# Performance work log

Hardware: AMD Instinct MI355X
Metric: run time of the kernel (lower is better)

Reference implementation:

```python
import jax, jax.numpy as jnp
import numpy as np

D = 1024      # hidden_size
H = 16        # num_heads
HD = D // H   # head_dim = 64
FF = 4096     # intermediate_size
DEPTH = 2
S = 2048      # packed sequence length
NSEG = 4     # number of image segments
EPS = 1e-6


def setup_inputs() -> dict:
    key = jax.random.key(0)
    ks = jax.random.split(key, 8)
    hidden_states = jax.random.normal(ks[0], (S, D), jnp.float32)
    cu_seqlens = jnp.arange(NSEG + 1, dtype=jnp.int32) * (S // NSEG)
    # rotary embedding like RiceRotaryEmbedding(head_dim//2): freqs of dim HD//4
    # per spatial axis, h/w concatenated -> HD//2, then duplicated -> HD
    inv_freq = 1.0 / (10000.0 ** (jnp.arange(0, HD // 2, 2, dtype=jnp.float32) / (HD // 2)))
    pos = jnp.arange(S, dtype=jnp.float32)
    freqs = jnp.outer(pos, inv_freq)                       # [S, HD//4]
    emb = jnp.concatenate([freqs] * 4, axis=-1)            # [S, HD]
    cos, sin = jnp.cos(emb), jnp.sin(emb)

    def w(k, shape, fan):
        return jax.random.normal(k, shape, jnp.float32) / np.sqrt(fan)

    return {
        "hidden_states": hidden_states,
        "cu_seqlens": cu_seqlens,
        "cos": cos,
        "sin": sin,
        "ln1_g": jnp.ones((DEPTH, D), jnp.float32),
        "ln1_b": jnp.zeros((DEPTH, D), jnp.float32),
        "qkv_w": w(ks[1], (DEPTH, D, 3 * D), D),
        "qkv_b": jnp.zeros((DEPTH, 3 * D), jnp.float32),
        "proj_w": w(ks[2], (DEPTH, D, D), D),
        "proj_b": jnp.zeros((DEPTH, D), jnp.float32),
        "ln2_g": jnp.ones((DEPTH, D), jnp.float32),
        "ln2_b": jnp.zeros((DEPTH, D), jnp.float32),
        "fc1_w": w(ks[3], (DEPTH, D, FF), D),
        "fc1_b": jnp.zeros((DEPTH, FF), jnp.float32),
        "fc2_w": w(ks[4], (DEPTH, FF, D), FF),
        "fc2_b": jnp.zeros((DEPTH, D), jnp.float32),
    }


def _ln(x, g, b):
    m = jnp.mean(x, axis=-1, keepdims=True)
    v = jnp.mean(jnp.square(x - m), axis=-1, keepdims=True)
    return (x - m) / jnp.sqrt(v + EPS) * g + b


def _rotate_half(x):
    x1, x2 = jnp.split(x, 2, axis=-1)
    return jnp.concatenate([-x2, x1], axis=-1)


def reference(hidden_states, cu_seqlens, cos, sin,
              ln1_g, ln1_b, qkv_w, qkv_b, proj_w, proj_b,
              ln2_g, ln2_b, fc1_w, fc1_b, fc2_w, fc2_b):
    S_, D_ = hidden_states.shape
    # segment id per token from cu_seqlens -> block-diagonal additive mask
    seg = jnp.searchsorted(cu_seqlens[1:], jnp.arange(S_, dtype=jnp.int32), side="right")
    neg = jnp.finfo(jnp.float32).min
    bias = jnp.where(seg[:, None] == seg[None, :], 0.0, neg)   # [S, S]
    cos_e = cos[:, None, :]  # broadcast over heads, [S,1,HD]
    sin_e = sin[:, None, :]
    scale = 1.0 / np.sqrt(HD)

    x = hidden_states
    for i in range(DEPTH):
        # --- attention ---
        h = _ln(x, ln1_g[i], ln1_b[i])
        qkv = h @ qkv_w[i] + qkv_b[i]                           # [S, 3D]
        q, k, v = [t.reshape(S_, H, HD) for t in jnp.split(qkv, 3, axis=-1)]
        q = q * cos_e + _rotate_half(q) * sin_e
        k = k * cos_e + _rotate_half(k) * sin_e
        scores = jnp.einsum("shd,thd->hst", q, k) * scale + bias  # [H,S,S]
        w_ = jax.nn.softmax(scores.astype(jnp.float32), axis=-1)
        ao = jnp.einsum("hst,thd->shd", w_, v).reshape(S_, D_)
        x = x + ao @ proj_w[i] + proj_b[i]
        # --- mlp ---
        h2 = _ln(x, ln2_g[i], ln2_b[i])
        x = x + jax.nn.gelu(h2 @ fc1_w[i] + fc1_b[i], approximate=False) @ fc2_w[i] + fc2_b[i]
    return x
```

## Files before the change

kernel.cpp:

```cpp
#include <hip/hip_runtime.h>
#include <hip/hip_bf16.h>
#include <math.h>

#define Dm 1024
#define Hn 16
#define HDm 64
#define FFm 4096
#define Sn 2048
#define SEG 512
#define EPSV 1e-6f

typedef __attribute__((ext_vector_type(4))) float f32x4;
typedef __attribute__((ext_vector_type(8))) short s16x8;
typedef __attribute__((ext_vector_type(4))) short s16x4;

__device__ inline short f2bf(float f) {
  __hip_bfloat16 h = __float2bfloat16(f);
  short s;
  __builtin_memcpy(&s, &h, 2);
  return s;
}
__device__ inline float bf2f(short s) {
  unsigned u = ((unsigned)(unsigned short)s) << 16;
  float f;
  __builtin_memcpy(&f, &u, 4);
  return f;
}

__device__ inline float wred_sum(float v) {
#pragma unroll
  for (int m = 32; m > 0; m >>= 1) v += __shfl_xor(v, m, 64);
  return v;
}
__device__ inline float wred_max(float v) {
#pragma unroll
  for (int m = 32; m > 0; m >>= 1) v = fmaxf(v, __shfl_xor(v, m, 64));
  return v;
}

__device__ inline void gld16(const short* g, short* lds_base) {
  __builtin_amdgcn_global_load_lds(
      (const __attribute__((address_space(1))) void*)g,
      (__attribute__((address_space(3))) void*)lds_base, 16, 0, 0);
}

__global__ __launch_bounds__(256) void ln_kernel(const float* __restrict__ x,
                                                 const float* __restrict__ g,
                                                 const float* __restrict__ b,
                                                 short* __restrict__ out) {
  const int row = blockIdx.x;
  const int tid = threadIdx.x;
  f32x4 v = *reinterpret_cast<const f32x4*>(x + (size_t)row * Dm + tid * 4);
  float s1 = v.x + v.y + v.z + v.w;
  float s2 = v.x * v.x + v.y * v.y + v.z * v.z + v.w * v.w;
  s1 = wred_sum(s1);
  s2 = wred_sum(s2);
  __shared__ float t1[4], t2[4];
  if ((tid & 63) == 0) { t1[tid >> 6] = s1; t2[tid >> 6] = s2; }
  __syncthreads();
  s1 = t1[0] + t1[1] + t1[2] + t1[3];
  s2 = t2[0] + t2[1] + t2[2] + t2[3];
  const float mean = s1 * (1.0f / Dm);
  const float var = s2 * (1.0f / Dm) - mean * mean;
  const float rstd = rsqrtf(var + EPSV);
  f32x4 gv = *reinterpret_cast<const f32x4*>(g + tid * 4);
  f32x4 bv = *reinterpret_cast<const f32x4*>(b + tid * 4);
  s16x4 o;
#pragma unroll
  for (int j = 0; j < 4; ++j)
    o[j] = f2bf((v[j] - mean) * rstd * gv[j] + bv[j]);
  *reinterpret_cast<s16x4*>(out + (size_t)row * Dm + tid * 4) = o;
}

template <int SPLIT>
__global__ __launch_bounds__(256) void redln_kernel(const float* __restrict__ pb,
                                                    const float* __restrict__ bias,
                                                    const float* __restrict__ res,
                                                    const float* __restrict__ g,
                                                    const float* __restrict__ b,
                                                    float* __restrict__ xout,
                                                    short* __restrict__ h) {
  const int row = blockIdx.x;
  const int tid = threadIdx.x;
  const size_t idx = (size_t)row * Dm + tid * 4;
  f32x4 o = *reinterpret_cast<const f32x4*>(res + idx);
  o += *reinterpret_cast<const f32x4*>(bias + tid * 4);
#pragma unroll
  for (int s = 0; s < SPLIT; ++s)
    o += *reinterpret_cast<const f32x4*>(pb + (size_t)s * Sn * Dm + idx);
  *reinterpret_cast<f32x4*>(xout + idx) = o;
  float s1 = o.x + o.y + o.z + o.w;
  float s2 = o.x * o.x + o.y * o.y + o.z * o.z + o.w * o.w;
  s1 = wred_sum(s1);
  s2 = wred_sum(s2);
  __shared__ float t1[4], t2[4];
  if ((tid & 63) == 0) { t1[tid >> 6] = s1; t2[tid >> 6] = s2; }
  __syncthreads();
  s1 = t1[0] + t1[1] + t1[2] + t1[3];
  s2 = t2[0] + t2[1] + t2[2] + t2[3];
  const float mean = s1 * (1.0f / Dm);
  const float var = s2 * (1.0f / Dm) - mean * mean;
  const float rstd = rsqrtf(var + EPSV);
  f32x4 gv = *reinterpret_cast<const f32x4*>(g + tid * 4);
  f32x4 bv = *reinterpret_cast<const f32x4*>(b + tid * 4);
  s16x4 ho;
#pragma unroll
  for (int j = 0; j < 4; ++j)
    ho[j] = f2bf((o[j] - mean) * rstd * gv[j] + bv[j]);
  *reinterpret_cast<s16x4*>(h + idx) = ho;
}

template <int SPLIT>
__global__ __launch_bounds__(256) void redln_bf(const short* __restrict__ pb,
                                                const float* __restrict__ bias,
                                                const float* __restrict__ res,
                                                const float* __restrict__ g,
                                                const float* __restrict__ b,
                                                float* __restrict__ xout,
                                                short* __restrict__ h) {
  const int row = blockIdx.x;
  const int tid = threadIdx.x;
  const size_t idx = (size_t)row * Dm + tid * 4;
  f32x4 o = *reinterpret_cast<const f32x4*>(res + idx);
  o += *reinterpret_cast<const f32x4*>(bias + tid * 4);
#pragma unroll
  for (int s = 0; s < SPLIT; ++s) {
    s16x4 v = *reinterpret_cast<const s16x4*>(pb + (size_t)s * Sn * Dm + idx);
#pragma unroll
    for (int j = 0; j < 4; ++j) o[j] += bf2f(v[j]);
  }
  *reinterpret_cast<f32x4*>(xout + idx) = o;
  float s1 = o.x + o.y + o.z + o.w;
  float s2 = o.x * o.x + o.y * o.y + o.z * o.z + o.w * o.w;
  s1 = wred_sum(s1);
  s2 = wred_sum(s2);
  __shared__ float t1[4], t2[4];
  if ((tid & 63) == 0) { t1[tid >> 6] = s1; t2[tid >> 6] = s2; }
  __syncthreads();
  s1 = t1[0] + t1[1] + t1[2] + t1[3];
  s2 = t2[0] + t2[1] + t2[2] + t2[3];
  const float mean = s1 * (1.0f / Dm);
  const float var = s2 * (1.0f / Dm) - mean * mean;
  const float rstd = rsqrtf(var + EPSV);
  f32x4 gv = *reinterpret_cast<const f32x4*>(g + tid * 4);
  f32x4 bv = *reinterpret_cast<const f32x4*>(b + tid * 4);
  s16x4 ho;
#pragma unroll
  for (int j = 0; j < 4; ++j)
    ho[j] = f2bf((o[j] - mean) * rstd * gv[j] + bv[j]);
  *reinterpret_cast<s16x4*>(h + idx) = ho;
}

template <int SPLIT>
__global__ __launch_bounds__(256) void fcred_bf(const short* __restrict__ pb,
                                                const float* __restrict__ bias,
                                                const float* __restrict__ res,
                                                float* __restrict__ out) {
  const size_t i = ((size_t)blockIdx.x * 256 + threadIdx.x) * 4;
  f32x4 o = *reinterpret_cast<const f32x4*>(res + i);
  o += *reinterpret_cast<const f32x4*>(bias + (i & (Dm - 1)));
#pragma unroll
  for (int s = 0; s < SPLIT; ++s) {
    s16x4 v = *reinterpret_cast<const s16x4*>(pb + (size_t)s * Sn * Dm + i);
#pragma unroll
    for (int j = 0; j < 4; ++j) o[j] += bf2f(v[j]);
  }
  *reinterpret_cast<f32x4*>(out + i) = o;
}

__global__ __launch_bounds__(256) void wt_kernel(const float* __restrict__ W,
                                                 short* __restrict__ Wt,
                                                 int K, int N, int ldw) {
  __shared__ float t[32][33];
  const int n0 = blockIdx.x * 32, k0 = blockIdx.y * 32;
  const int tx = threadIdx.x & 31, ty = threadIdx.x >> 5;
#pragma unroll
  for (int r = 0; r < 32; r += 8)
    t[r + ty][tx] = W[(size_t)(k0 + r + ty) * ldw + n0 + tx];
  __syncthreads();
#pragma unroll
  for (int r = 0; r < 32; r += 8)
    Wt[(size_t)(n0 + r + ty) * K + k0 + tx] = f2bf(t[tx][r + ty]);
}

__global__ __launch_bounds__(256) void wtb_kernel(const short* __restrict__ V,
                                                  short* __restrict__ Vt,
                                                  int K, int N, int ldv) {
  __shared__ short t[32][34];
  const int n0 = blockIdx.x * 32, k0 = blockIdx.y * 32;
  const int tx = threadIdx.x & 31, ty = threadIdx.x >> 5;
#pragma unroll
  for (int r = 0; r < 32; r += 8)
    t[r + ty][tx] = V[(size_t)(k0 + r + ty) * ldv + n0 + tx];
  __syncthreads();
#pragma unroll
  for (int r = 0; r < 32; r += 8)
    Vt[(size_t)(n0 + r + ty) * K + k0 + tx] = t[tx][r + ty];
}

__global__ __launch_bounds__(512) void qksoft_kernel(const short* __restrict__ qkvb,
                                                     short* __restrict__ probs) {
  __shared__ short Qs[128 * 64];
  __shared__ short Ks[512 * 64];
  __shared__ float red[128][4];
  const int tid = threadIdx.x;
  const int lane = tid & 63;
  const int wave = tid >> 6;
  const int wm = wave >> 2, wn = wave & 3;
  const int l15 = lane & 15, lg = lane >> 4, rx = l15 & 7;
  const int qblk = blockIdx.x;
  const int z = blockIdx.y;
  const int seg = z & 3, head = z >> 2;

  const int srow = tid >> 3;
  const int sch = ((tid & 7) ^ (srow & 7)) * 8;

  const short* Qg = qkvb + (size_t)(seg * SEG + qblk * 128 + srow) * 3072 +
                    head * HDm + sch;
  const short* Kg = qkvb + (size_t)(seg * SEG + srow) * 3072 + Dm +
                    head * HDm + sch;
#pragma unroll
  for (int j = 0; j < 2; ++j)
    gld16(Qg + (size_t)(j * 64) * 3072, &Qs[(j * 64 + wave * 8) * 64]);
#pragma unroll
  for (int j = 0; j < 8; ++j)
    gld16(Kg + (size_t)(j * 64) * 3072, &Ks[(j * 64 + wave * 8) * 64]);
  __syncthreads();

  f32x4 acc[4][8] = {};
#pragma unroll
  for (int kc = 0; kc < 8; kc += 4) {
    s16x8 af[4], bf8[8];
#pragma unroll
    for (int f = 0; f < 4; ++f)
      af[f] = *reinterpret_cast<const s16x8*>(
          &Qs[(wm * 64 + f * 16 + l15) * 64 + (((lg + kc) ^ rx) << 3)]);
#pragma unroll
    for (int f = 0; f < 8; ++f)
      bf8[f] = *reinterpret_cast<const s16x8*>(
          &Ks[(wn * 128 + f * 16 + l15) * 64 + (((lg + kc) ^ rx) << 3)]);
#pragma unroll
    for (int fi = 0; fi < 4; ++fi)
#pragma unroll
      for (int fj = 0; fj < 8; ++fj)
        acc[fi][fj] = __builtin_amdgcn_mfma_f32_16x16x32_bf16(
            af[fi], bf8[fj], acc[fi][fj], 0, 0, 0);
  }

  float Ms[4][4];
#pragma unroll
  for (int fi = 0; fi < 4; ++fi) {
#pragma unroll
    for (int r = 0; r < 4; ++r) {
      float m = acc[fi][0][r];
#pragma unroll
      for (int fj = 1; fj < 8; ++fj) m = fmaxf(m, acc[fi][fj][r]);
#pragma unroll
      for (int d = 1; d < 16; d <<= 1) m = fmaxf(m, __shfl_xor(m, d, 64));
      Ms[fi][r] = m;
    }
  }
  if (l15 == 0) {
#pragma unroll
    for (int fi = 0; fi < 4; ++fi)
#pragma unroll
      for (int r = 0; r < 4; ++r)
        red[wm * 64 + fi * 16 + lg * 4 + r][wn] = Ms[fi][r];
  }
  __syncthreads();
#pragma unroll
  for (int fi = 0; fi < 4; ++fi) {
#pragma unroll
    for (int r = 0; r < 4; ++r) {
      const int row = wm * 64 + fi * 16 + lg * 4 + r;
      float m = fmaxf(fmaxf(red[row][0], red[row][1]),
                      fmaxf(red[row][2], red[row][3]));
      Ms[fi][r] = m * 0.125f;
    }
  }
  __syncthreads();

  float Sv[4][4];
#pragma unroll
  for (int fi = 0; fi < 4; ++fi) {
#pragma unroll
    for (int r = 0; r < 4; ++r) {
      float s = 0.f;
#pragma unroll
      for (int fj = 0; fj < 8; ++fj) {
        float pv = __expf(acc[fi][fj][r] * 0.125f - Ms[fi][r]);
        acc[fi][fj][r] = pv;
        s += pv;
      }
#pragma unroll
      for (int d = 1; d < 16; d <<= 1) s += __shfl_xor(s, d, 64);
      Sv[fi][r] = s;
    }
  }
  if (l15 == 0) {
#pragma unroll
    for (int fi = 0; fi < 4; ++fi)
#pragma unroll
      for (int r = 0; r < 4; ++r)
        red[wm * 64 + fi * 16 + lg * 4 + r][wn] = Sv[fi][r];
  }
  __syncthreads();

  short* pb = probs + (size_t)z * SEG * SEG + (size_t)qblk * 128 * SEG;
#pragma unroll
  for (int fi = 0; fi < 4; ++fi) {
#pragma unroll
    for (int r = 0; r < 4; ++r) {
      const int row = wm * 64 + fi * 16 + lg * 4 + r;
      const float inv =
          1.0f / (red[row][0] + red[row][1] + red[row][2] + red[row][3]);
#pragma unroll
      for (int fj = 0; fj < 8; ++fj) {
        const int col = wn * 128 + fj * 16 + l15;
        pb[(size_t)row * SEG + col] = f2bf(acc[fi][fj][r] * inv);
      }
    }
  }
}

struct GemmArgs {
  const short* A; int lda;
  const short* B; int ldb;
  void* C; int ldc;
  int M, N, K;
  const float* bias;
  const float* cosb; const float* sinb;
  float scale;
};

template <int BM, int BN, int SPLIT, int MODE>
__global__ __launch_bounds__(256) void gemm6(GemmArgs p) {
  constexpr int WN = 2;
  constexpr int WM = 2;
  constexpr int FI = BM / WM / 16;
  constexpr int FJ = BN / WN / 16;
  const int z = blockIdx.z;
  const short* A = p.A;
  const short* B = p.B;
  char* Cb = (char*)p.C;
  int kbase = 0, nkt = p.K >> 6;
  int tileM, tileN;
  if (MODE == 2) {
    tileM = blockIdx.y * BM;
    tileN = blockIdx.x * BN;
  } else {
    const int gx = gridDim.x;
    const int nwg = gx * gridDim.y;
    const int orig = blockIdx.y * gx + blockIdx.x;
    const int sid = (orig & 7) * (nwg >> 3) + (orig >> 3);
    tileM = (sid / gx) * BM;
    tileN = (sid % gx) * BN;
  }
  if (MODE == 2) {
    const int seg = z & 3, hh = z >> 2;
    A += (size_t)z * SEG * SEG;
    B += (size_t)(hh * HDm) * p.ldb + seg * SEG;
    Cb += ((size_t)seg * SEG * Dm + (size_t)hh * HDm) * 2;
  } else if (MODE == 3 || MODE == 6) {
    kbase = z * (p.K / SPLIT);
    nkt = (p.K / SPLIT) >> 6;
    Cb += (size_t)z * p.M * p.N * ((MODE == 3) ? 4 : 2);
  }
  __shared__ short As[BM * 64];
  __shared__ short Bs[BN * 64];
  const int tid = threadIdx.x;
  const int lane = tid & 63;
  const int wave = tid >> 6;
  const int l15 = lane & 15;
  const int lg = lane >> 4;
  const int rx = l15 & 7;
  const int wr = (wave / WN) * (BM / WM);
  const int wc = (wave % WN) * (BN / WN);
  const int srow = lane >> 3;
  const int scol = ((lane & 7) ^ srow) * 8;

  f32x4 acc[FI][FJ] = {};

  const short* Ag = A + (size_t)(tileM + wave * 8 + srow) * p.lda + scol + kbase;
  const short* Bg = B + (size_t)(tileN + wave * 8 + srow) * p.ldb + scol + kbase;

  for (int kt = 0; kt < nkt; ++kt) {
    const int k0 = kt * 64;
#pragma unroll
    for (int j = 0; j < BM / 32; ++j)
      gld16(Ag + (size_t)(j * 32) * p.lda + k0, &As[(j * 32 + wave * 8) * 64]);
#pragma unroll
    for (int j = 0; j < BN / 32; ++j)
      gld16(Bg + (size_t)(j * 32) * p.ldb + k0, &Bs[(j * 32 + wave * 8) * 64]);
    __syncthreads();
#pragma unroll
    for (int kk = 0; kk < 64; kk += 32) {
      const int kkc = kk >> 3;
      s16x8 af[FI], bfr[FJ];
#pragma unroll
      for (int f = 0; f < FI; ++f)
        af[f] = *reinterpret_cast<const s16x8*>(
            &As[(wr + f * 16 + l15) * 64 + (((lg + kkc) ^ rx) << 3)]);
#pragma unroll
      for (int f = 0; f < FJ; ++f)
        bfr[f] = *reinterpret_cast<const s16x8*>(
            &Bs[(wc + f * 16 + l15) * 64 + (((lg + kkc) ^ rx) << 3)]);
#pragma unroll
      for (int fi = 0; fi < FI; ++fi)
#pragma unroll
        for (int fj = 0; fj < FJ; ++fj)
          acc[fi][fj] = __builtin_amdgcn_mfma_f32_16x16x32_bf16(
              af[fi], bfr[fj], acc[fi][fj], 0, 0, 0);
    }
    __syncthreads();
  }

  if (MODE == 4) {
    short* Cs = (short*)Cb;
    const bool isqk = (tileN + wc) < 2048;
#pragma unroll
    for (int fi = 0; fi < FI; ++fi) {
#pragma unroll
      for (int fj = 0; fj < FJ; ++fj) {
#pragma unroll
        for (int r = 0; r < 4; ++r) {
          const int row = tileM + wr + fi * 16 + lg * 4 + r;
          const int col = tileN + wc + fj * 16 + l15;
          float a0 = acc[fi][fj][r] + p.bias[col];
          float vout;
          if (isqk) {
            float a1 = acc[fi][fj ^ 2][r] + p.bias[col ^ 32];
            const int dl = fj * 16 + l15;
            const float c = p.cosb[(size_t)row * HDm + dl];
            const float sn = p.sinb[(size_t)row * HDm + dl];
            vout = (fj < 2) ? (a0 * c - a1 * sn) : (a0 * c + a1 * sn);
          } else {
            vout = a0;
          }
          Cs[(size_t)row * p.ldc + col] = f2bf(vout);
        }
      }
    }
    return;
  }

#pragma unroll
  for (int fi = 0; fi < FI; ++fi) {
#pragma unroll
    for (int fj = 0; fj < FJ; ++fj) {
#pragma unroll
      for (int r = 0; r < 4; ++r) {
        const int row = tileM + wr + fi * 16 + lg * 4 + r;
        const int col = tileN + wc + fj * 16 + l15;
        float v = acc[fi][fj][r] * p.scale;
        if (MODE == 5) {
          v += p.bias[col];
          v = 0.5f * v * (1.0f + erff(v * 0.70710678118654752f));
        }
        if (MODE == 2 || MODE == 5 || MODE == 6)
          reinterpret_cast<short*>(Cb)[(size_t)row * p.ldc + col] = f2bf(v);
        else
          reinterpret_cast<float*>(Cb)[(size_t)row * p.ldc + col] = v;
      }
    }
  }
}

extern "C" void kernel_launch(void* const* d_in, const int* in_sizes, int n_in,
                              void* d_out, int out_size, void* d_ws, size_t ws_size,
                              hipStream_t stream) {
  const float* x0 = (const float*)d_in[0];
  const float* cosb = (const float*)d_in[2];
  const float* sinb = (const float*)d_in[3];
  const float* ln1_g = (const float*)d_in[4];
  const float* ln1_b = (const float*)d_in[5];
  const float* qkv_w = (const float*)d_in[6];
  const float* qkv_b = (const float*)d_in[7];
  const float* proj_w = (const float*)d_in[8];
  const float* proj_b = (const float*)d_in[9];
  const float* ln2_g = (const float*)d_in[10];
  const float* ln2_b = (const float*)d_in[11];
  const float* fc1_w = (const float*)d_in[12];
  const float* fc1_b = (const float*)d_in[13];
  const float* fc2_w = (const float*)d_in[14];
  const float* fc2_b = (const float*)d_in[15];

  char* ws = (char*)d_ws;
  size_t off = 0;
  auto alloc = [&](size_t bytes) {
    void* p = ws + off;
    off += (bytes + 255) & ~(size_t)255;
    return p;
  };
  short* wqkvT = (short*)alloc((size_t)2 * 3072 * 1024 * 2);
  short* wprojT = (short*)alloc((size_t)2 * 1024 * 1024 * 2);
  short* wfc1T = (short*)alloc((size_t)2 * 4096 * 1024 * 2);
  short* wfc2T = (short*)alloc((size_t)2 * 1024 * 4096 * 2);
  float* xbuf = (float*)alloc((size_t)Sn * Dm * 4);
  short* hbuf = (short*)alloc((size_t)Sn * Dm * 2);
  short* qkvb = (short*)alloc((size_t)Sn * 3 * Dm * 2);
  short* probs = (short*)alloc((size_t)64 * SEG * SEG * 2);
  float* pbuf = (float*)alloc((size_t)4 * Sn * Dm * 4);
  short* pbufS = (short*)pbuf;
  short* ao = (short*)alloc((size_t)Sn * Dm * 2);
  short* ffn = (short*)alloc((size_t)Sn * FFm * 2);
  short* vT = ffn;
  (void)ws_size; (void)in_sizes; (void)n_in; (void)out_size;

  for (int i = 0; i < 2; ++i) {
    wt_kernel<<<dim3(96, 32), 256, 0, stream>>>(
        qkv_w + (size_t)i * Dm * 3072, wqkvT + (size_t)i * 3072 * Dm, Dm, 3072, 3072);
    wt_kernel<<<dim3(32, 32), 256, 0, stream>>>(
        proj_w + (size_t)i * Dm * Dm, wprojT + (size_t)i * Dm * Dm, Dm, Dm, Dm);
    wt_kernel<<<dim3(128, 32), 256, 0, stream>>>(
        fc1_w + (size_t)i * Dm * FFm, wfc1T + (size_t)i * FFm * Dm, Dm, FFm, FFm);
    wt_kernel<<<dim3(32, 128), 256, 0, stream>>>(
        fc2_w + (size_t)i * FFm * Dm, wfc2T + (size_t)i * Dm * FFm, FFm, Dm, Dm);
  }

  ln_kernel<<<dim3(Sn), 256, 0, stream>>>(x0, ln1_g, ln1_b, hbuf);

  for (int i = 0; i < 2; ++i) {
    const float* xin = i ? (const float*)xbuf : x0;

    {
      GemmArgs p = {};
      p.A = hbuf; p.lda = Dm;
      p.B = wqkvT + (size_t)i * 3072 * Dm; p.ldb = Dm;
      p.C = qkvb; p.ldc = 3 * Dm;
      p.M = Sn; p.N = 3 * Dm; p.K = Dm;
      p.bias = qkv_b + i * 3 * Dm; p.cosb = cosb; p.sinb = sinb; p.scale = 1.0f;
      gemm6<64, 128, 1, 4><<<dim3(24, 32, 1), 256, 0, stream>>>(p);
    }

    wtb_kernel<<<dim3(32, 64), 256, 0, stream>>>(qkvb + 2 * Dm, vT, Sn, Dm, 3 * Dm);

    qksoft_kernel<<<dim3(4, 64), 512, 0, stream>>>(qkvb, probs);

    {
      GemmArgs p = {};
      p.A = probs; p.lda = SEG;
      p.B = vT; p.ldb = Sn;
      p.C = ao; p.ldc = Dm;
      p.M = SEG; p.N = HDm; p.K = SEG; p.scale = 1.0f;
      gemm6<64, 64, 1, 2><<<dim3(1, 8, 64), 256, 0, stream>>>(p);
    }

    {
      GemmArgs p = {};
      p.A = ao; p.lda = Dm;
      p.B = wprojT + (size_t)i * Dm * Dm; p.ldb = Dm;
      p.C = pbuf; p.ldc = Dm;
      p.M = Sn; p.N = Dm; p.K = Dm; p.scale = 1.0f;
      gemm6<64, 64, 2, 3><<<dim3(16, 32, 2), 256, 0, stream>>>(p);
    }
    redln_kernel<2><<<dim3(Sn), 256, 0, stream>>>(
        pbuf, proj_b + i * Dm, xin, ln2_g + i * Dm, ln2_b + i * Dm, xbuf, hbuf);

    {
      GemmArgs p = {};
      p.A = hbuf; p.lda = Dm;
      p.B = wfc1T + (size_t)i * FFm * Dm; p.ldb = Dm;
      p.C = ffn; p.ldc = FFm;
      p.M = Sn; p.N = FFm; p.K = Dm;
      p.bias = fc1_b + i * FFm; p.scale = 1.0f;
      gemm6<64, 128, 1, 5><<<dim3(32, 32, 1), 256, 0, stream>>>(p);
    }

    {
      GemmArgs p = {};
      p.A = ffn; p.lda = FFm;
      p.B = wfc2T + (size_t)i * Dm * FFm; p.ldb = FFm;
      p.C = pbufS; p.ldc = Dm;
      p.M = Sn; p.N = Dm; p.K = FFm; p.scale = 1.0f;
      gemm6<64, 128, 4, 6><<<dim3(8, 32, 4), 256, 0, stream>>>(p);
    }
    if (i == 0) {
      redln_bf<4><<<dim3(Sn), 256, 0, stream>>>(
          pbufS, fc2_b, xbuf, ln1_g + Dm, ln1_b + Dm, xbuf, hbuf);
    } else {
      fcred_bf<4><<<dim3(Sn * Dm / 1024), 256, 0, stream>>>(
          pbufS, fc2_b + Dm, xbuf, (float*)d_out);
    }
  }
}
```

Measured before the change: 321.4 us.

## Fuse P·V into attention softmax kernel and store proj split-K partials as bf16

```diff
diff --git a/kernel.cpp b/kernel.cpp
--- a/kernel.cpp
+++ b/kernel.cpp
@@ -30,11 +30,6 @@
 __device__ inline float wred_sum(float v) {
 #pragma unroll
   for (int m = 32; m > 0; m >>= 1) v += __shfl_xor(v, m, 64);
-  return v;
-}
-__device__ inline float wred_max(float v) {
-#pragma unroll
-  for (int m = 32; m > 0; m >>= 1) v = fmaxf(v, __shfl_xor(v, m, 64));
   return v;
 }
 
@@ -73,44 +68,6 @@
 }
 
 template <int SPLIT>
-__global__ __launch_bounds__(256) void redln_kernel(const float* __restrict__ pb,
-                                                    const float* __restrict__ bias,
-                                                    const float* __restrict__ res,
-                                                    const float* __restrict__ g,
-                                                    const float* __restrict__ b,
-                                                    float* __restrict__ xout,
-                                                    short* __restrict__ h) {
-  const int row = blockIdx.x;
-  const int tid = threadIdx.x;
-  const size_t idx = (size_t)row * Dm + tid * 4;
-  f32x4 o = *reinterpret_cast<const f32x4*>(res + idx);
-  o += *reinterpret_cast<const f32x4*>(bias + tid * 4);
-#pragma unroll
-  for (int s = 0; s < SPLIT; ++s)
-    o += *reinterpret_cast<const f32x4*>(pb + (size_t)s * Sn * Dm + idx);
-  *reinterpret_cast<f32x4*>(xout + idx) = o;
-  float s1 = o.x + o.y + o.z + o.w;
-  float s2 = o.x * o.x + o.y * o.y + o.z * o.z + o.w * o.w;
-  s1 = wred_sum(s1);
-  s2 = wred_sum(s2);
-  __shared__ float t1[4], t2[4];
-  if ((tid & 63) == 0) { t1[tid >> 6] = s1; t2[tid >> 6] = s2; }
-  __syncthreads();
-  s1 = t1[0] + t1[1] + t1[2] + t1[3];
-  s2 = t2[0] + t2[1] + t2[2] + t2[3];
-  const float mean = s1 * (1.0f / Dm);
-  const float var = s2 * (1.0f / Dm) - mean * mean;
-  const float rstd = rsqrtf(var + EPSV);
-  f32x4 gv = *reinterpret_cast<const f32x4*>(g + tid * 4);
-  f32x4 bv = *reinterpret_cast<const f32x4*>(b + tid * 4);
-  s16x4 ho;
-#pragma unroll
-  for (int j = 0; j < 4; ++j)
-    ho[j] = f2bf((o[j] - mean) * rstd * gv[j] + bv[j]);
-  *reinterpret_cast<s16x4*>(h + idx) = ho;
-}
-
-template <int SPLIT>
 __global__ __launch_bounds__(256) void redln_bf(const short* __restrict__ pb,
                                                 const float* __restrict__ bias,
                                                 const float* __restrict__ res,
@@ -198,10 +155,12 @@
     Vt[(size_t)(n0 + r + ty) * K + k0 + tx] = t[tx][r + ty];
 }
 
-__global__ __launch_bounds__(512) void qksoft_kernel(const short* __restrict__ qkvb,
-                                                     short* __restrict__ probs) {
+__global__ __launch_bounds__(512) void qksoftpv_kernel(const short* __restrict__ qkvb,
+                                                       const short* __restrict__ vT,
+                                                       short* __restrict__ ao) {
   __shared__ short Qs[128 * 64];
   __shared__ short Ks[512 * 64];
+  __shared__ short Vs[64 * 512];
   __shared__ float red[128][4];
   const int tid = threadIdx.x;
   const int lane = tid & 63;
@@ -225,7 +184,18 @@
 #pragma unroll
   for (int j = 0; j < 8; ++j)
     gld16(Kg + (size_t)(j * 64) * 3072, &Ks[(j * 64 + wave * 8) * 64]);
-  __syncthreads();
+  {
+    const short* Vg = vT + (size_t)(head * 64) * Sn + seg * SEG;
+#pragma unroll
+    for (int j = 0; j < 8; ++j) {
+      const int d = j * 8 + wave;
+      const int c = (lane & ~7) | ((lane & 7) ^ (d & 7));
+      gld16(Vg + (size_t)d * Sn + c * 8, &Vs[d * 512]);
+    }
+  }
+  asm volatile("s_waitcnt vmcnt(8)" ::: "memory");
+  __builtin_amdgcn_s_barrier();
+  __builtin_amdgcn_sched_barrier(0);
 
   f32x4 acc[4][8] = {};
 #pragma unroll
@@ -306,20 +276,56 @@
   }
   __syncthreads();
 
-  short* pb = probs + (size_t)z * SEG * SEG + (size_t)qblk * 128 * SEG;
-#pragma unroll
-  for (int fi = 0; fi < 4; ++fi) {
-#pragma unroll
-    for (int r = 0; r < 4; ++r) {
-      const int row = wm * 64 + fi * 16 + lg * 4 + r;
-      const float inv =
-          1.0f / (red[row][0] + red[row][1] + red[row][2] + red[row][3]);
-#pragma unroll
-      for (int fj = 0; fj < 8; ++fj) {
-        const int col = wn * 128 + fj * 16 + l15;
-        pb[(size_t)row * SEG + col] = f2bf(acc[fi][fj][r] * inv);
+  asm volatile("s_waitcnt vmcnt(0)" ::: "memory");
+
+  short* Ps = Ks;
+  f32x4 pv[4] = {};
+  const int q2 = wave * 16 + l15;
+  const int sxr = (q2 ^ (q2 >> 3)) & 7;
+#pragma unroll
+  for (int kh = 0; kh < 2; ++kh) {
+    if ((wn >> 1) == kh) {
+#pragma unroll
+      for (int fi = 0; fi < 4; ++fi)
+#pragma unroll
+        for (int fj = 0; fj < 8; ++fj)
+#pragma unroll
+          for (int r = 0; r < 4; ++r) {
+            const int q = wm * 64 + fi * 16 + lg * 4 + r;
+            const int kp = (wn & 1) * 128 + fj * 16 + l15;
+            const int c = kp >> 3;
+            const int sxw = (q ^ (q >> 3)) & 7;
+            const int cs = (c & 24) | ((c & 7) ^ sxw);
+            Ps[q * 256 + cs * 8 + (kp & 7)] = f2bf(acc[fi][fj][r]);
+          }
+    }
+    __syncthreads();
+#pragma unroll
+    for (int ks = 0; ks < 8; ++ks) {
+      const int ca = ks * 4 + lg;
+      const int csa = (ca & 24) | ((ca & 7) ^ sxr);
+      s16x8 pa = *reinterpret_cast<const s16x8*>(&Ps[q2 * 256 + csa * 8]);
+#pragma unroll
+      for (int fj = 0; fj < 4; ++fj) {
+        const int d = fj * 16 + l15;
+        const int cb = kh * 32 + ks * 4 + lg;
+        const int csb = (cb & ~7) | ((cb & 7) ^ (d & 7));
+        s16x8 pb = *reinterpret_cast<const s16x8*>(&Vs[d * 512 + csb * 8]);
+        pv[fj] = __builtin_amdgcn_mfma_f32_16x16x32_bf16(pa, pb, pv[fj], 0, 0, 0);
       }
     }
+    __syncthreads();
+  }
+
+#pragma unroll
+  for (int r = 0; r < 4; ++r) {
+    const int q2o = wave * 16 + lg * 4 + r;
+    const float inv =
+        1.0f / (red[q2o][0] + red[q2o][1] + red[q2o][2] + red[q2o][3]);
+    const size_t rowg = (size_t)(seg * SEG + qblk * 128 + q2o) * Dm + head * 64;
+#pragma unroll
+    for (int fj = 0; fj < 4; ++fj)
+      ao[rowg + fj * 16 + l15] = f2bf(pv[fj][r] * inv);
   }
 }
 
@@ -344,24 +350,13 @@
   const short* B = p.B;
   char* Cb = (char*)p.C;
   int kbase = 0, nkt = p.K >> 6;
-  int tileM, tileN;
-  if (MODE == 2) {
-    tileM = blockIdx.y * BM;
-    tileN = blockIdx.x * BN;
-  } else {
-    const int gx = gridDim.x;
-    const int nwg = gx * gridDim.y;
-    const int orig = blockIdx.y * gx + blockIdx.x;
-    const int sid = (orig & 7) * (nwg >> 3) + (orig >> 3);
-    tileM = (sid / gx) * BM;
-    tileN = (sid % gx) * BN;
-  }
-  if (MODE == 2) {
-    const int seg = z & 3, hh = z >> 2;
-    A += (size_t)z * SEG * SEG;
-    B += (size_t)(hh * HDm) * p.ldb + seg * SEG;
-    Cb += ((size_t)seg * SEG * Dm + (size_t)hh * HDm) * 2;
-  } else if (MODE == 3 || MODE == 6) {
+  const int gx = gridDim.x;
+  const int nwg = gx * gridDim.y;
+  const int orig = blockIdx.y * gx + blockIdx.x;
+  const int sid = (orig & 7) * (nwg >> 3) + (orig >> 3);
+  const int tileM = (sid / gx) * BM;
+  const int tileN = (sid % gx) * BN;
+  if (MODE == 3 || MODE == 6) {
     kbase = z * (p.K / SPLIT);
     nkt = (p.K / SPLIT) >> 6;
     Cb += (size_t)z * p.M * p.N * ((MODE == 3) ? 4 : 2);
@@ -457,7 +452,7 @@
           v += p.bias[col];
           v = 0.5f * v * (1.0f + erff(v * 0.70710678118654752f));
         }
-        if (MODE == 2 || MODE == 5 || MODE == 6)
+        if (MODE == 5 || MODE == 6)
           reinterpret_cast<short*>(Cb)[(size_t)row * p.ldc + col] = f2bf(v);
         else
           reinterpret_cast<float*>(Cb)[(size_t)row * p.ldc + col] = v;
@@ -499,7 +494,6 @@
   float* xbuf = (float*)alloc((size_t)Sn * Dm * 4);
   short* hbuf = (short*)alloc((size_t)Sn * Dm * 2);
   short* qkvb = (short*)alloc((size_t)Sn * 3 * Dm * 2);
-  short* probs = (short*)alloc((size_t)64 * SEG * SEG * 2);
   float* pbuf = (float*)alloc((size_t)4 * Sn * Dm * 4);
   short* pbufS = (short*)pbuf;
   short* ao = (short*)alloc((size_t)Sn * Dm * 2);
@@ -535,27 +529,18 @@
 
     wtb_kernel<<<dim3(32, 64), 256, 0, stream>>>(qkvb + 2 * Dm, vT, Sn, Dm, 3 * Dm);
 
-    qksoft_kernel<<<dim3(4, 64), 512, 0, stream>>>(qkvb, probs);
-
-    {
-      GemmArgs p = {};
-      p.A = probs; p.lda = SEG;
-      p.B = vT; p.ldb = Sn;
-      p.C = ao; p.ldc = Dm;
-      p.M = SEG; p.N = HDm; p.K = SEG; p.scale = 1.0f;
-      gemm6<64, 64, 1, 2><<<dim3(1, 8, 64), 256, 0, stream>>>(p);
-    }
+    qksoftpv_kernel<<<dim3(4, 64), 512, 0, stream>>>(qkvb, vT, ao);
 
     {
       GemmArgs p = {};
       p.A = ao; p.lda = Dm;
       p.B = wprojT + (size_t)i * Dm * Dm; p.ldb = Dm;
-      p.C = pbuf; p.ldc = Dm;
+      p.C = pbufS; p.ldc = Dm;
       p.M = Sn; p.N = Dm; p.K = Dm; p.scale = 1.0f;
-      gemm6<64, 64, 2, 3><<<dim3(16, 32, 2), 256, 0, stream>>>(p);
-    }
-    redln_kernel<2><<<dim3(Sn), 256, 0, stream>>>(
-        pbuf, proj_b + i * Dm, xin, ln2_g + i * Dm, ln2_b + i * Dm, xbuf, hbuf);
+      gemm6<64, 64, 2, 6><<<dim3(16, 32, 2), 256, 0, stream>>>(p);
+    }
+    redln_bf<2><<<dim3(Sn), 256, 0, stream>>>(
+        pbufS, proj_b + i * Dm, xin, ln2_g + i * Dm, ln2_b + i * Dm, xbuf, hbuf);
 
     {
       GemmArgs p = {};
```

Measured after the change: 302.8 us. 1.06x faster.
